# Performance work log

Measured on AMD Instinct MI355X. Metric: run time of the kernel, lower is better.

The kernel has to match this reference:

```python
import jax, jax.numpy as jnp
import numpy as np

K = 3
K2 = K * K
EPS = 1e-5


def conv2d(x, w, stride=1, pad=1):
    return jax.lax.conv_general_dilated(
        x, w, (stride, stride), [(pad, pad), (pad, pad)],
        dimension_numbers=("NCHW", "OIHW", "NCHW"))


def bilinear_sample(x, py, px):
    """x: [B,C,H,W]; py,px: [B,Ho,Wo,K2] float sample coords.
    Zero padding outside bounds (torchvision deform_conv2d semantics).
    Returns [B,C,Ho,Wo,K2]."""
    B, C, H, W = x.shape
    Ho, Wo = py.shape[1], py.shape[2]
    y0 = jnp.floor(py)
    x0 = jnp.floor(px)
    wy1 = py - y0
    wx1 = px - x0
    x_flat = x.reshape(B, C, H * W)

    def gather(yi, xi):
        valid = (yi >= 0) & (yi < H) & (xi >= 0) & (xi < W)
        yc = jnp.clip(yi, 0, H - 1).astype(jnp.int32)
        xc = jnp.clip(xi, 0, W - 1).astype(jnp.int32)
        idx = (yc * W + xc).reshape(B, 1, -1)          # [B,1,N]
        v = jnp.take_along_axis(x_flat, idx, axis=2)   # [B,C,N]
        return v * valid.reshape(B, 1, -1).astype(x.dtype)

    w00 = ((1 - wy1) * (1 - wx1)).reshape(B, 1, -1)
    w01 = ((1 - wy1) * wx1).reshape(B, 1, -1)
    w10 = (wy1 * (1 - wx1)).reshape(B, 1, -1)
    w11 = (wy1 * wx1).reshape(B, 1, -1)
    val = (w00 * gather(y0, x0) + w01 * gather(y0, x0 + 1)
           + w10 * gather(y0 + 1, x0) + w11 * gather(y0 + 1, x0 + 1))
    return val.reshape(B, C, Ho, Wo, K2)


def deform_conv_bn_relu(x, d, offset_w, conv_w, gamma, beta):
    # offset branch: 3x3 conv on d, clamp to [-1,1]
    offset = jnp.clip(conv2d(d, offset_w, 1, 1), -1.0, 1.0)  # [B,2*K2,H,W]
    B, Cin, H, W = x.shape
    Cout = conv_w.shape[0]
    off = offset.reshape(B, K2, 2, H, W)
    dy = off[:, :, 0].transpose(0, 2, 3, 1)  # [B,H,W,K2]
    dx = off[:, :, 1].transpose(0, 2, 3, 1)
    kh = (jnp.arange(K2) // K).astype(jnp.float32)
    kw = (jnp.arange(K2) % K).astype(jnp.float32)
    # sample coords: out pixel + kernel tap - padding + learned offset
    py = (jnp.arange(H, dtype=jnp.float32)[None, :, None, None] - 1.0
          + kh[None, None, None, :] + dy)
    px = (jnp.arange(W, dtype=jnp.float32)[None, None, :, None] - 1.0
          + kw[None, None, None, :] + dx)
    sampled = bilinear_sample(x, py, px)  # [B,Cin,H,W,K2]
    out = jnp.einsum('bchwk,ock->bohw', sampled,
                     conv_w.reshape(Cout, Cin, K2))
    # BatchNorm2d (training forward: biased batch stats) + ReLU
    mean = out.mean(axis=(0, 2, 3))
    var = out.var(axis=(0, 2, 3))
    inv = gamma / jnp.sqrt(var + EPS)
    out = (out - mean[None, :, None, None]) * inv[None, :, None, None] \
        + beta[None, :, None, None]
    out = jax.nn.relu(out)
    return out, offset


def setup_inputs() -> dict:
    key = jax.random.key(0)
    k1, k2, k3, k4 = jax.random.split(key, 4)
    B, C, H, W = 4, 64, 160, 160
    Cout, offC = 64, 64
    x = jax.random.normal(k1, (B, C, H, W), dtype=jnp.float32)
    d = jax.random.normal(k2, (B, offC, H, W), dtype=jnp.float32)
    # torch zero-inits offset_conv; use small random weights so the
    # bilinear gather path is actually exercised with fractional offsets
    offset_w = jax.random.normal(k3, (2 * K2, offC, K, K), dtype=jnp.float32) * 0.01
    conv_w = jax.random.normal(k4, (Cout, C, K, K), dtype=jnp.float32) * (1.0 / np.sqrt(C * K2))
    gamma = jnp.ones((Cout,), dtype=jnp.float32)
    beta = jnp.zeros((Cout,), dtype=jnp.float32)
    return {"x": x, "d": d, "offset_w": offset_w, "conv_w": conv_w,
            "gamma": gamma, "beta": beta}


def reference(x, d, offset_w, conv_w, gamma, beta):
    return deform_conv_bn_relu(x, d, offset_w, conv_w, gamma, beta)
```

## Files before the change

### kernel.cpp

```cpp
#include <hip/hip_runtime.h>
#include <hip/hip_bf16.h>

#define BB 4
#define HH 160
#define WW 160
#define HWD (HH * WW)
#define OUT_ELEMS (BB * 64 * HWD)
#define OFF_ELEMS (BB * 18 * HWD)
#define EPSBN 1e-5f
#define CHSTRIDE (8 * HWD)
#define NSLOT 256

typedef __attribute__((ext_vector_type(8))) short bf16x8;
typedef __attribute__((ext_vector_type(4))) float f32x4;

__device__ inline unsigned pack2bf(float a, float b) {
  __hip_bfloat162 h2 = __float22bfloat162_rn(float2{a, b});
  unsigned u;
  __builtin_memcpy(&u, &h2, 4);
  return u;
}
__device__ inline unsigned short bf16bits(float a) {
  __hip_bfloat16 h = __float2bfloat16(a);
  unsigned short u;
  __builtin_memcpy(&u, &h, 2);
  return u;
}

__device__ inline void ldsbar() {
  asm volatile("s_waitcnt lgkmcnt(0)" ::: "memory");
  __builtin_amdgcn_s_barrier();
}

__device__ inline void tile_map(int blk, int& b, int& ty0, int& tx0) {
  int t = (blk & 7) * 200 + (blk >> 3);
  b = t / 400;
  int r = t % 400;
  ty0 = (r / 10) * 4;
  tx0 = (r % 10) * 16;
}

__global__ void prep_kernel(const float* __restrict__ cw,
                            const float* __restrict__ ow,
                            unsigned short* __restrict__ Bp,
                            unsigned short* __restrict__ B2p,
                            float* __restrict__ part) {
  int i = blockIdx.x * 256 + threadIdx.x;
  if (i < 32768) part[i] = 0.f;
  if (i < 49152) {
    int j = i & 7, l = (i >> 3) & 63, rest = i >> 9;
    int ki = rest % 24, nt = rest / 24;
    int kp = ki * 32 + ((l >> 4) << 3) + j;
    int chunk = kp / 96, kq = kp % 96;
    int t = kq >> 3, c = kq & 7;
    int n = nt * 16 + (l & 15);
    float v = (t < 9) ? cw[n * 576 + (chunk * 8 + c) * 9 + t] : 0.f;
    Bp[i] = bf16bits(v);
  }
  if (i < 24576) {
    int j = i & 7, l = (i >> 3) & 63, rest = i >> 9;
    int ki = rest % 24, nt = rest / 24;
    int kp = ki * 32 + ((l >> 4) << 3) + j;
    int chunk = kp / 96, kq = kp % 96;
    int t = kq >> 3, c = kq & 7;
    int n = nt * 16 + (l & 15);
    float v = (t < 9 && n < 18) ? ow[n * 576 + (chunk * 8 + c) * 9 + t] : 0.f;
    B2p[i] = bf16bits(v);
  }
}

__global__ __launch_bounds__(256, 4) void fused_kernel(
    const float* __restrict__ x, const float* __restrict__ d,
    const bf16x8* __restrict__ Bp, const bf16x8* __restrict__ B2p,
    float* __restrict__ out, float* __restrict__ off_out,
    float* __restrict__ part) {
  int b, ty0, tx0;
  tile_map(blockIdx.x, b, ty0, tx0);
  const int tid = threadIdx.x;
  const int wv = tid >> 6, lane = tid & 63;
  const int lo = lane >> 4, li = lane & 15;
  const int px = li, py = wv;
  const int h = ty0 + py, w = tx0 + px;

  __shared__ float patch[189 * 12];
  __shared__ bf16x8 Af[768];
  __shared__ float offs_s[64 * 18];

  int goff2[2], laddr2[2];
  bool inr2[2], ok2[2];
#pragma unroll
  for (int i = 0; i < 2; ++i) {
    int idx = tid + i * 256;
    int ch4 = idx / 189, p = idx % 189;
    int r = p / 21, col = p % 21;
    int gy = ty0 - 2 + r, gx = tx0 - 2 + col;
    inr2[i] = idx < 378;
    ok2[i] = inr2[i] && gy >= 0 && gy < HH && gx >= 0 && gx < WW;
    goff2[i] = ((b * 64 + ch4 * 4) * HH + gy) * WW + gx;
    laddr2[i] = p * 12 + ch4 * 4;
  }

  f32x4 acc0{0.f, 0.f, 0.f, 0.f}, acc1{0.f, 0.f, 0.f, 0.f};
  const int ntA = wv >> 1, mh = wv & 1;
  {
    int poff[3];
    bool tre[3];
#pragma unroll
    for (int kk = 0; kk < 3; ++kk) {
      int t = kk * 4 + lo;
      tre[kk] = (t < 9);
      poff[kk] = tre[kk] ? ((py + t / 3) * 18 + px + t % 3) : 0;
    }

    int goff1 = 0, laddr1 = 0;
    bool inr1 = tid < 216, ok1 = false;
    {
      int ch4 = tid / 108, p = tid % 108;
      int r = p / 18, col = p % 18;
      int gy = ty0 - 1 + r, gx = tx0 - 1 + col;
      ok1 = inr1 && gy >= 0 && gy < HH && gx >= 0 && gx < WW;
      goff1 = ((b * 64 + ch4 * 4) * HH + gy) * WW + gx;
      laddr1 = p * 12 + ch4 * 4;
    }
    float4 g1 = make_float4(0.f, 0.f, 0.f, 0.f);
    if (ok1) {
      const float* pp = d + goff1;
      g1 = make_float4(pp[0], pp[HWD], pp[2 * HWD], pp[3 * HWD]);
    }

    for (int chunk = 0; chunk < 8; ++chunk) {
      bf16x8 bw0 = B2p[((ntA * 24 + chunk * 3 + 0) << 6) + lane];
      bf16x8 bw1 = B2p[((ntA * 24 + chunk * 3 + 1) << 6) + lane];
      bf16x8 bw2 = B2p[((ntA * 24 + chunk * 3 + 2) << 6) + lane];
      if (inr1) *(float4*)&patch[laddr1] = g1;
      ldsbar();
      int nco = ((chunk < 7) ? (chunk + 1) : 7) * CHSTRIDE;
      if (ok1) {
        const float* pp = d + goff1 + nco;
        g1 = make_float4(pp[0], pp[HWD], pp[2 * HWD], pp[3 * HWD]);
      }
#pragma unroll
      for (int kk = 0; kk < 3; ++kk) {
        union { bf16x8 v; unsigned u[4]; } a;
        if (tre[kk]) {
          const float* q = patch + poff[kk] * 12;
          float4 c0 = *(const float4*)(q);
          float4 c1 = *(const float4*)(q + 4);
          a.u[0] = pack2bf(c0.x, c0.y);
          a.u[1] = pack2bf(c0.z, c0.w);
          a.u[2] = pack2bf(c1.x, c1.y);
          a.u[3] = pack2bf(c1.z, c1.w);
        } else {
          a.u[0] = a.u[1] = a.u[2] = a.u[3] = 0u;
        }
        Af[((wv * 3 + kk) << 6) + lane] = a.v;
      }
      ldsbar();
#pragma unroll
      for (int kk = 0; kk < 3; ++kk) {
        bf16x8 bw = (kk == 0) ? bw0 : (kk == 1) ? bw1 : bw2;
        acc0 = __builtin_amdgcn_mfma_f32_16x16x32_bf16(
            Af[(((mh * 2) * 3 + kk) << 6) + lane], bw, acc0, 0, 0, 0);
        acc1 = __builtin_amdgcn_mfma_f32_16x16x32_bf16(
            Af[(((mh * 2 + 1) * 3 + kk) << 6) + lane], bw, acc1, 0, 0, 0);
      }
    }
  }

  float4 gv4[2];
#pragma unroll
  for (int i = 0; i < 2; ++i) {
    gv4[i] = make_float4(0.f, 0.f, 0.f, 0.f);
    if (ok2[i]) {
      const float* pp = x + goff2[i];
      gv4[i] = make_float4(pp[0], pp[HWD], pp[2 * HWD], pp[3 * HWD]);
    }
  }

  {
    const int n = ntA * 16 + li;
    if (n < 18) {
#pragma unroll
      for (int f = 0; f < 2; ++f) {
        int mf = mh * 2 + f;
        f32x4 a = f ? acc1 : acc0;
        float* po =
            off_out + ((b * 18 + n) * HH + ty0 + mf) * WW + tx0 + lo * 4;
        float4 v;
        v.x = fminf(1.f, fmaxf(-1.f, a[0]));
        v.y = fminf(1.f, fmaxf(-1.f, a[1]));
        v.z = fminf(1.f, fmaxf(-1.f, a[2]));
        v.w = fminf(1.f, fmaxf(-1.f, a[3]));
        *(float4*)po = v;
        int pix = mf * 16 + lo * 4;
        offs_s[(pix + 0) * 18 + n] = v.x;
        offs_s[(pix + 1) * 18 + n] = v.y;
        offs_s[(pix + 2) * 18 + n] = v.z;
        offs_s[(pix + 3) * 18 + n] = v.w;
      }
    }
  }
  ldsbar();

  int bs[3];
  float W00[3], W01[3], W10[3], W11[3];
  bool tre[3];
#pragma unroll
  for (int kk = 0; kk < 3; ++kk) {
    int t = kk * 4 + lo;
    tre[kk] = (t < 9);
    if (tre[kk]) {
      float dy = offs_s[(py * 16 + px) * 18 + 2 * t];
      float dx = offs_s[(py * 16 + px) * 18 + 2 * t + 1];
      float pyf = (float)(h - 1 + t / 3) + dy;
      float pxf = (float)(w - 1 + t % 3) + dx;
      float y0 = floorf(pyf), x0 = floorf(pxf);
      float wy = pyf - y0, wx = pxf - x0;
      bs[kk] = ((int)y0 - (ty0 - 2)) * 21 + ((int)x0 - (tx0 - 2));
      W00[kk] = (1.f - wy) * (1.f - wx);
      W01[kk] = (1.f - wy) * wx;
      W10[kk] = wy * (1.f - wx);
      W11[kk] = wy * wx;
    } else {
      bs[kk] = 0;
      W00[kk] = W01[kk] = W10[kk] = W11[kk] = 0.f;
    }
  }

  f32x4 acc[4];
#pragma unroll
  for (int i = 0; i < 4; ++i) acc[i] = f32x4{0.f, 0.f, 0.f, 0.f};
  const int nt = wv;

  for (int chunk = 0; chunk < 8; ++chunk) {
    bf16x8 bw0 = Bp[((nt * 24 + chunk * 3 + 0) << 6) + lane];
    bf16x8 bw1 = Bp[((nt * 24 + chunk * 3 + 1) << 6) + lane];
    bf16x8 bw2 = Bp[((nt * 24 + chunk * 3 + 2) << 6) + lane];
#pragma unroll
    for (int i = 0; i < 2; ++i)
      if (inr2[i]) *(float4*)&patch[laddr2[i]] = gv4[i];
    ldsbar();
    int nco = ((chunk < 7) ? (chunk + 1) : 7) * CHSTRIDE;
#pragma unroll
    for (int i = 0; i < 2; ++i) {
      if (ok2[i]) {
        const float* pp = x + goff2[i] + nco;
        gv4[i] = make_float4(pp[0], pp[HWD], pp[2 * HWD], pp[3 * HWD]);
      }
    }
#pragma unroll
    for (int kk = 0; kk < 3; ++kk) {
      union { bf16x8 v; unsigned u[4]; } a;
      if (tre[kk]) {
        const float* q = patch + bs[kk] * 12;
        float4 p00a = *(const float4*)(q);
        float4 p00b = *(const float4*)(q + 4);
        float4 p01a = *(const float4*)(q + 12);
        float4 p01b = *(const float4*)(q + 16);
        float4 p10a = *(const float4*)(q + 252);
        float4 p10b = *(const float4*)(q + 256);
        float4 p11a = *(const float4*)(q + 264);
        float4 p11b = *(const float4*)(q + 268);
        float w0 = W00[kk], w1 = W01[kk], w2 = W10[kk], w3 = W11[kk];
        float v0 = fmaf(w3, p11a.x, fmaf(w2, p10a.x, fmaf(w1, p01a.x, w0 * p00a.x)));
        float v1 = fmaf(w3, p11a.y, fmaf(w2, p10a.y, fmaf(w1, p01a.y, w0 * p00a.y)));
        float v2 = fmaf(w3, p11a.z, fmaf(w2, p10a.z, fmaf(w1, p01a.z, w0 * p00a.z)));
        float v3 = fmaf(w3, p11a.w, fmaf(w2, p10a.w, fmaf(w1, p01a.w, w0 * p00a.w)));
        float v4 = fmaf(w3, p11b.x, fmaf(w2, p10b.x, fmaf(w1, p01b.x, w0 * p00b.x)));
        float v5 = fmaf(w3, p11b.y, fmaf(w2, p10b.y, fmaf(w1, p01b.y, w0 * p00b.y)));
        float v6 = fmaf(w3, p11b.z, fmaf(w2, p10b.z, fmaf(w1, p01b.z, w0 * p00b.z)));
        float v7 = fmaf(w3, p11b.w, fmaf(w2, p10b.w, fmaf(w1, p01b.w, w0 * p00b.w)));
        a.u[0] = pack2bf(v0, v1);
        a.u[1] = pack2bf(v2, v3);
        a.u[2] = pack2bf(v4, v5);
        a.u[3] = pack2bf(v6, v7);
      } else {
        a.u[0] = a.u[1] = a.u[2] = a.u[3] = 0u;
      }
      Af[((wv * 3 + kk) << 6) + lane] = a.v;
    }
    ldsbar();
#pragma unroll
    for (int kk = 0; kk < 3; ++kk) {
      bf16x8 bw = (kk == 0) ? bw0 : (kk == 1) ? bw1 : bw2;
#pragma unroll
      for (int mf = 0; mf < 4; ++mf)
        acc[mf] = __builtin_amdgcn_mfma_f32_16x16x32_bf16(
            Af[((mf * 3 + kk) << 6) + lane], bw, acc[mf], 0, 0, 0);
    }
  }
  const int n = nt * 16 + li;
  float s = 0.f, s2 = 0.f;
#pragma unroll
  for (int mf = 0; mf < 4; ++mf) {
    float* po = out + ((b * 64 + n) * HH + ty0 + mf) * WW + tx0 + lo * 4;
    *(float4*)po = make_float4(acc[mf][0], acc[mf][1], acc[mf][2], acc[mf][3]);
#pragma unroll
    for (int r = 0; r < 4; ++r) {
      float v = acc[mf][r];
      s += v;
      s2 = fmaf(v, v, s2);
    }
  }
  s += __shfl_xor(s, 16);  s += __shfl_xor(s, 32);
  s2 += __shfl_xor(s2, 16); s2 += __shfl_xor(s2, 32);
  if (lo == 0) {
    int slot = blockIdx.x & (NSLOT - 1);
    atomicAdd(&part[n * NSLOT + slot], s);
    atomicAdd(&part[(64 + n) * NSLOT + slot], s2);
  }
}

__global__ __launch_bounds__(256) void reduce_kernel(
    const float* __restrict__ part, double* __restrict__ sums) {
  const int j = blockIdx.x;
  __shared__ double sh[256];
  sh[threadIdx.x] = (double)part[j * NSLOT + threadIdx.x];
  __syncthreads();
  for (int t = 128; t > 0; t >>= 1) {
    if (threadIdx.x < t) sh[threadIdx.x] += sh[threadIdx.x + t];
    __syncthreads();
  }
  if (threadIdx.x == 0) sums[j] = sh[0];
}

__global__ __launch_bounds__(256) void bnapply_kernel(
    float* __restrict__ out, const double* __restrict__ sums,
    const float* __restrict__ gamma, const float* __restrict__ beta) {
  const int i = blockIdx.x * 256 + threadIdx.x;
  if (i >= OUT_ELEMS / 4) return;
  const int o = (i / (HWD / 4)) & 63;
  const float n_inv = 1.0f / (float)(BB * HWD);
  float mean = (float)sums[o] * n_inv;
  float var = (float)sums[64 + o] * n_inv - mean * mean;
  float inv = gamma[o] * rsqrtf(var + EPSBN);
  float bt = beta[o];
  float4 v = ((float4*)out)[i];
  v.x = fmaxf(0.f, (v.x - mean) * inv + bt);
  v.y = fmaxf(0.f, (v.y - mean) * inv + bt);
  v.z = fmaxf(0.f, (v.z - mean) * inv + bt);
  v.w = fmaxf(0.f, (v.w - mean) * inv + bt);
  ((float4*)out)[i] = v;
}

extern "C" void kernel_launch(void* const* d_in, const int* in_sizes, int n_in,
                              void* d_out, int out_size, void* d_ws, size_t ws_size,
                              hipStream_t stream) {
  const float* x = (const float*)d_in[0];
  const float* d = (const float*)d_in[1];
  const float* ow = (const float*)d_in[2];
  const float* cw = (const float*)d_in[3];
  const float* gamma = (const float*)d_in[4];
  const float* beta = (const float*)d_in[5];

  float* out = (float*)d_out;
  float* off_out = out + OUT_ELEMS;

  double* sums = (double*)d_ws;
  unsigned short* Bp = (unsigned short*)((char*)d_ws + 1024);
  unsigned short* B2p = Bp + 49152;
  float* part = (float*)(B2p + 24576);

  prep_kernel<<<192, 256, 0, stream>>>(cw, ow, Bp, B2p, part);

  fused_kernel<<<1600, 256, 0, stream>>>(x, d, (const bf16x8*)Bp,
                                         (const bf16x8*)B2p, out, off_out,
                                         part);

  reduce_kernel<<<128, 256, 0, stream>>>(part, sums);
  bnapply_kernel<<<(OUT_ELEMS / 4 + 255) / 256, 256, 0, stream>>>(
      out, sums, gamma, beta);
}
```

Measured before the change: 157.9 us.

## Switch to fp16 MFMA with fp16 LDS patch and packed fp16 bilinear math

Result: faster. 154.3 us (-2.3%).

```diff
diff --git a/kernel.cpp b/kernel.cpp
--- a/kernel.cpp
+++ b/kernel.cpp
@@ -11,20 +11,31 @@
 #define CHSTRIDE (8 * HWD)
 #define NSLOT 256
 
-typedef __attribute__((ext_vector_type(8))) short bf16x8;
+typedef __attribute__((ext_vector_type(8))) _Float16 f16x8;
 typedef __attribute__((ext_vector_type(4))) float f32x4;
 
-__device__ inline unsigned pack2bf(float a, float b) {
-  __hip_bfloat162 h2 = __float22bfloat162_rn(float2{a, b});
-  unsigned u;
-  __builtin_memcpy(&u, &h2, 4);
-  return u;
-}
-__device__ inline unsigned short bf16bits(float a) {
-  __hip_bfloat16 h = __float2bfloat16(a);
+__device__ inline unsigned short f16bits(float a) {
+  _Float16 h = (_Float16)a;
   unsigned short u;
   __builtin_memcpy(&u, &h, 2);
   return u;
+}
+
+__device__ inline unsigned pkrtz(float a, float b) {
+  __fp16 __attribute__((ext_vector_type(2))) t =
+      __builtin_amdgcn_cvt_pkrtz(a, b);
+  unsigned u;
+  __builtin_memcpy(&u, &t, 4);
+  return u;
+}
+
+__device__ inline f16x8 load8cvt(const float* pp) {
+  union { f16x8 v; unsigned u[4]; } r;
+  r.u[0] = pkrtz(pp[0], pp[HWD]);
+  r.u[1] = pkrtz(pp[2 * HWD], pp[3 * HWD]);
+  r.u[2] = pkrtz(pp[4 * HWD], pp[5 * HWD]);
+  r.u[3] = pkrtz(pp[6 * HWD], pp[7 * HWD]);
+  return r.v;
 }
 
 __device__ inline void ldsbar() {
@@ -55,7 +66,7 @@
     int t = kq >> 3, c = kq & 7;
     int n = nt * 16 + (l & 15);
     float v = (t < 9) ? cw[n * 576 + (chunk * 8 + c) * 9 + t] : 0.f;
-    Bp[i] = bf16bits(v);
+    Bp[i] = f16bits(v);
   }
   if (i < 24576) {
     int j = i & 7, l = (i >> 3) & 63, rest = i >> 9;
@@ -65,13 +76,13 @@
     int t = kq >> 3, c = kq & 7;
     int n = nt * 16 + (l & 15);
     float v = (t < 9 && n < 18) ? ow[n * 576 + (chunk * 8 + c) * 9 + t] : 0.f;
-    B2p[i] = bf16bits(v);
+    B2p[i] = f16bits(v);
   }
 }
 
 __global__ __launch_bounds__(256, 4) void fused_kernel(
     const float* __restrict__ x, const float* __restrict__ d,
-    const bf16x8* __restrict__ Bp, const bf16x8* __restrict__ B2p,
+    const f16x8* __restrict__ Bp, const f16x8* __restrict__ B2p,
     float* __restrict__ out, float* __restrict__ off_out,
     float* __restrict__ part) {
   int b, ty0, tx0;
@@ -82,22 +93,22 @@
   const int px = li, py = wv;
   const int h = ty0 + py, w = tx0 + px;
 
-  __shared__ float patch[189 * 12];
-  __shared__ bf16x8 Af[768];
+  __shared__ __align__(16) _Float16 patch[189 * 8];
+  __shared__ f16x8 Af[768];
   __shared__ float offs_s[64 * 18];
 
-  int goff2[2], laddr2[2];
-  bool inr2[2], ok2[2];
-#pragma unroll
-  for (int i = 0; i < 2; ++i) {
-    int idx = tid + i * 256;
-    int ch4 = idx / 189, p = idx % 189;
+  const f16x8 zero8 = {(_Float16)0, (_Float16)0, (_Float16)0, (_Float16)0,
+                       (_Float16)0, (_Float16)0, (_Float16)0, (_Float16)0};
+
+  int goff2 = 0, laddr2 = 0;
+  bool inr2 = tid < 189, ok2 = false;
+  {
+    int p = tid;
     int r = p / 21, col = p % 21;
     int gy = ty0 - 2 + r, gx = tx0 - 2 + col;
-    inr2[i] = idx < 378;
-    ok2[i] = inr2[i] && gy >= 0 && gy < HH && gx >= 0 && gx < WW;
-    goff2[i] = ((b * 64 + ch4 * 4) * HH + gy) * WW + gx;
-    laddr2[i] = p * 12 + ch4 * 4;
+    ok2 = inr2 && gy >= 0 && gy < HH && gx >= 0 && gx < WW;
+    goff2 = ((b * 64) * HH + gy) * WW + gx;
+    laddr2 = p * 8;
   }
 
   f32x4 acc0{0.f, 0.f, 0.f, 0.f}, acc1{0.f, 0.f, 0.f, 0.f};
@@ -113,69 +124,45 @@
     }
 
     int goff1 = 0, laddr1 = 0;
-    bool inr1 = tid < 216, ok1 = false;
+    bool inr1 = tid < 108, ok1 = false;
     {
-      int ch4 = tid / 108, p = tid % 108;
+      int p = tid;
       int r = p / 18, col = p % 18;
       int gy = ty0 - 1 + r, gx = tx0 - 1 + col;
       ok1 = inr1 && gy >= 0 && gy < HH && gx >= 0 && gx < WW;
-      goff1 = ((b * 64 + ch4 * 4) * HH + gy) * WW + gx;
-      laddr1 = p * 12 + ch4 * 4;
-    }
-    float4 g1 = make_float4(0.f, 0.f, 0.f, 0.f);
-    if (ok1) {
-      const float* pp = d + goff1;
-      g1 = make_float4(pp[0], pp[HWD], pp[2 * HWD], pp[3 * HWD]);
-    }
+      goff1 = ((b * 64) * HH + gy) * WW + gx;
+      laddr1 = p * 8;
+    }
+    f16x8 g1 = zero8;
+    if (ok1) g1 = load8cvt(d + goff1);
 
     for (int chunk = 0; chunk < 8; ++chunk) {
-      bf16x8 bw0 = B2p[((ntA * 24 + chunk * 3 + 0) << 6) + lane];
-      bf16x8 bw1 = B2p[((ntA * 24 + chunk * 3 + 1) << 6) + lane];
-      bf16x8 bw2 = B2p[((ntA * 24 + chunk * 3 + 2) << 6) + lane];
-      if (inr1) *(float4*)&patch[laddr1] = g1;
+      f16x8 bw0 = B2p[((ntA * 24 + chunk * 3 + 0) << 6) + lane];
+      f16x8 bw1 = B2p[((ntA * 24 + chunk * 3 + 1) << 6) + lane];
+      f16x8 bw2 = B2p[((ntA * 24 + chunk * 3 + 2) << 6) + lane];
+      if (inr1) *(f16x8*)&patch[laddr1] = g1;
       ldsbar();
       int nco = ((chunk < 7) ? (chunk + 1) : 7) * CHSTRIDE;
-      if (ok1) {
-        const float* pp = d + goff1 + nco;
-        g1 = make_float4(pp[0], pp[HWD], pp[2 * HWD], pp[3 * HWD]);
-      }
+      if (ok1) g1 = load8cvt(d + goff1 + nco);
 #pragma unroll
       for (int kk = 0; kk < 3; ++kk) {
-        union { bf16x8 v; unsigned u[4]; } a;
-        if (tre[kk]) {
-          const float* q = patch + poff[kk] * 12;
-          float4 c0 = *(const float4*)(q);
-          float4 c1 = *(const float4*)(q + 4);
-          a.u[0] = pack2bf(c0.x, c0.y);
-          a.u[1] = pack2bf(c0.z, c0.w);
-          a.u[2] = pack2bf(c1.x, c1.y);
-          a.u[3] = pack2bf(c1.z, c1.w);
-        } else {
-          a.u[0] = a.u[1] = a.u[2] = a.u[3] = 0u;
-        }
-        Af[((wv * 3 + kk) << 6) + lane] = a.v;
+        f16x8 av = tre[kk] ? *(const f16x8*)(patch + poff[kk] * 8) : zero8;
+        Af[((wv * 3 + kk) << 6) + lane] = av;
       }
       ldsbar();
 #pragma unroll
       for (int kk = 0; kk < 3; ++kk) {
-        bf16x8 bw = (kk == 0) ? bw0 : (kk == 1) ? bw1 : bw2;
-        acc0 = __builtin_amdgcn_mfma_f32_16x16x32_bf16(
+        f16x8 bw = (kk == 0) ? bw0 : (kk == 1) ? bw1 : bw2;
+        acc0 = __builtin_amdgcn_mfma_f32_16x16x32_f16(
             Af[(((mh * 2) * 3 + kk) << 6) + lane], bw, acc0, 0, 0, 0);
-        acc1 = __builtin_amdgcn_mfma_f32_16x16x32_bf16(
+        acc1 = __builtin_amdgcn_mfma_f32_16x16x32_f16(
             Af[(((mh * 2 + 1) * 3 + kk) << 6) + lane], bw, acc1, 0, 0, 0);
       }
     }
   }
 
-  float4 gv4[2];
-#pragma unroll
-  for (int i = 0; i < 2; ++i) {
-    gv4[i] = make_float4(0.f, 0.f, 0.f, 0.f);
-    if (ok2[i]) {
-      const float* pp = x + goff2[i];
-      gv4[i] = make_float4(pp[0], pp[HWD], pp[2 * HWD], pp[3 * HWD]);
-    }
-  }
+  f16x8 gv = zero8;
+  if (ok2) gv = load8cvt(x + goff2);
 
   {
     const int n = ntA * 16 + li;
@@ -233,59 +220,41 @@
   const int nt = wv;
 
   for (int chunk = 0; chunk < 8; ++chunk) {
-    bf16x8 bw0 = Bp[((nt * 24 + chunk * 3 + 0) << 6) + lane];
-    bf16x8 bw1 = Bp[((nt * 24 + chunk * 3 + 1) << 6) + lane];
-    bf16x8 bw2 = Bp[((nt * 24 + chunk * 3 + 2) << 6) + lane];
-#pragma unroll
-    for (int i = 0; i < 2; ++i)
-      if (inr2[i]) *(float4*)&patch[laddr2[i]] = gv4[i];
+    f16x8 bw0 = Bp[((nt * 24 + chunk * 3 + 0) << 6) + lane];
+    f16x8 bw1 = Bp[((nt * 24 + chunk * 3 + 1) << 6) + lane];
+    f16x8 bw2 = Bp[((nt * 24 + chunk * 3 + 2) << 6) + lane];
+    if (inr2) *(f16x8*)&patch[laddr2] = gv;
     ldsbar();
     int nco = ((chunk < 7) ? (chunk + 1) : 7) * CHSTRIDE;
-#pragma unroll
-    for (int i = 0; i < 2; ++i) {
-      if (ok2[i]) {
-        const float* pp = x + goff2[i] + nco;
-        gv4[i] = make_float4(pp[0], pp[HWD], pp[2 * HWD], pp[3 * HWD]);
+    if (ok2) gv = load8cvt(x + goff2 + nco);
+#pragma unroll
+    for (int kk = 0; kk < 3; ++kk) {
+      f16x8 av;
+      if (tre[kk]) {
+        const _Float16* q = patch + bs[kk] * 8;
+        f16x8 p00 = *(const f16x8*)(q);
+        f16x8 p01 = *(const f16x8*)(q + 8);
+        f16x8 p10 = *(const f16x8*)(q + 168);
+        f16x8 p11 = *(const f16x8*)(q + 176);
+        _Float16 w0 = (_Float16)W00[kk], w1 = (_Float16)W01[kk];
+        _Float16 w2 = (_Float16)W10[kk], w3 = (_Float16)W11[kk];
+        f16x8 w0v = {w0, w0, w0, w0, w0, w0, w0, w0};
+        f16x8 w1v = {w1, w1, w1, w1, w1, w1, w1, w1};
+        f16x8 w2v = {w2, w2, w2, w2, w2, w2, w2, w2};
+        f16x8 w3v = {w3, w3, w3, w3, w3, w3, w3, w3};
+        av = p00 * w0v + p01 * w1v + p10 * w2v + p11 * w3v;
+      } else {
+        av = zero8;
       }
-    }
+      Af[((wv * 3 + kk) << 6) + lane] = av;
+    }
+    ldsbar();
 #pragma unroll
     for (int kk = 0; kk < 3; ++kk) {
-      union { bf16x8 v; unsigned u[4]; } a;
-      if (tre[kk]) {
-        const float* q = patch + bs[kk] * 12;
-        float4 p00a = *(const float4*)(q);
-        float4 p00b = *(const float4*)(q + 4);
-        float4 p01a = *(const float4*)(q + 12);
-        float4 p01b = *(const float4*)(q + 16);
-        float4 p10a = *(const float4*)(q + 252);
-        float4 p10b = *(const float4*)(q + 256);
-        float4 p11a = *(const float4*)(q + 264);
-        float4 p11b = *(const float4*)(q + 268);
-        float w0 = W00[kk], w1 = W01[kk], w2 = W10[kk], w3 = W11[kk];
-        float v0 = fmaf(w3, p11a.x, fmaf(w2, p10a.x, fmaf(w1, p01a.x, w0 * p00a.x)));
-        float v1 = fmaf(w3, p11a.y, fmaf(w2, p10a.y, fmaf(w1, p01a.y, w0 * p00a.y)));
-        float v2 = fmaf(w3, p11a.z, fmaf(w2, p10a.z, fmaf(w1, p01a.z, w0 * p00a.z)));
-        float v3 = fmaf(w3, p11a.w, fmaf(w2, p10a.w, fmaf(w1, p01a.w, w0 * p00a.w)));
-        float v4 = fmaf(w3, p11b.x, fmaf(w2, p10b.x, fmaf(w1, p01b.x, w0 * p00b.x)));
-        float v5 = fmaf(w3, p11b.y, fmaf(w2, p10b.y, fmaf(w1, p01b.y, w0 * p00b.y)));
-        float v6 = fmaf(w3, p11b.z, fmaf(w2, p10b.z, fmaf(w1, p01b.z, w0 * p00b.z)));
-        float v7 = fmaf(w3, p11b.w, fmaf(w2, p10b.w, fmaf(w1, p01b.w, w0 * p00b.w)));
-        a.u[0] = pack2bf(v0, v1);
-        a.u[1] = pack2bf(v2, v3);
-        a.u[2] = pack2bf(v4, v5);
-        a.u[3] = pack2bf(v6, v7);
-      } else {
-        a.u[0] = a.u[1] = a.u[2] = a.u[3] = 0u;
-      }
-      Af[((wv * 3 + kk) << 6) + lane] = a.v;
-    }
-    ldsbar();
-#pragma unroll
-    for (int kk = 0; kk < 3; ++kk) {
-      bf16x8 bw = (kk == 0) ? bw0 : (kk == 1) ? bw1 : bw2;
+      f16x8 bw = (kk == 0) ? bw0 : (kk == 1) ? bw1 : bw2;
 #pragma unroll
       for (int mf = 0; mf < 4; ++mf)
-        acc[mf] = __builtin_amdgcn_mfma_f32_16x16x32_bf16(
+        acc[mf] = __builtin_amdgcn_mfma_f32_16x16x32_f16(
             Af[((mf * 3 + kk) << 6) + lane], bw, acc[mf], 0, 0, 0);
     }
   }
@@ -363,8 +332,8 @@
 
   prep_kernel<<<192, 256, 0, stream>>>(cw, ow, Bp, B2p, part);
 
-  fused_kernel<<<1600, 256, 0, stream>>>(x, d, (const bf16x8*)Bp,
-                                         (const bf16x8*)B2p, out, off_out,
+  fused_kernel<<<1600, 256, 0, stream>>>(x, d, (const f16x8*)Bp,
+                                         (const f16x8*)B2p, out, off_out,
                                          part);
 
   reduce_kernel<<<128, 256, 0, stream>>>(part, sums);
```
